# Performance work log

Hardware: AMD Instinct MI355X
Metric: run time of the kernel (lower is better)

Reference implementation:

```python
import jax, jax.numpy as jnp
import numpy as np
import math

B, T, F, H = 8, 1024, 1024, 16
D = F // H

def setup_inputs() -> dict:
    key = jax.random.key(0)
    ks = jax.random.split(key, 6)
    s = 1.0 / math.sqrt(F)
    return {
        "qkv": jax.random.normal(ks[0], (B, T, F), dtype=jnp.float32),
        "key_padding_mask": jax.random.randint(ks[1], (B, T), 0, 2).astype(bool),
        "in_proj_w": jax.random.normal(ks[2], (3 * F, F), dtype=jnp.float32) * s,
        "in_proj_b": jax.random.normal(ks[3], (3 * F,), dtype=jnp.float32) * 0.02,
        "out_proj_w": jax.random.normal(ks[4], (F, F), dtype=jnp.float32) * s,
        "out_proj_b": jax.random.normal(ks[5], (F,), dtype=jnp.float32) * 0.02,
    }

def reference(qkv, key_padding_mask, in_proj_w, in_proj_b, out_proj_w, out_proj_b):
    b, t, f = qkv.shape
    h, d = H, f // H
    norm = jnp.asarray(math.sqrt(d), dtype=qkv.dtype)
    # fused QKV projection (torch Linear: x @ W.T + b)
    x = qkv @ in_proj_w.T + in_proj_b                     # [B, T, 3F]
    q, k, v = jnp.split(x, 3, axis=-1)
    q = q.reshape(b, t, h, d).transpose(0, 2, 1, 3)       # [B, H, T, D]
    k = k.reshape(b, t, h, d).transpose(0, 2, 1, 3)
    v = v.reshape(b, t, h, d).transpose(0, 2, 1, 3)
    dot = jnp.einsum("bhqd,bhkd->bhqk", q, k) / norm      # [B, H, T, T]
    dot = jnp.where(key_padding_mask[:, None, None, :], -jnp.inf, dot)
    alpha = jax.nn.softmax(dot, axis=-1)                  # [B, H, T, T]
    att = jnp.einsum("bhqk,bhkd->bhqd", alpha, v)         # [B, H, T, D]
    att = att.transpose(0, 2, 1, 3).reshape(b, t, f)      # [B, T, F]
    out = att @ out_proj_w.T + out_proj_b
    return (out, alpha)
```

## Files before the change

### kernel.cpp

```cpp
#include <hip/hip_runtime.h>
#include <math.h>

#define B_ 8
#define T_ 1024
#define F_ 1024
#define H_ 16
#define D_ 64

typedef __bf16 bf16x8 __attribute__((ext_vector_type(8)));
typedef float f32x4 __attribute__((ext_vector_type(4)));
typedef unsigned short u16x8 __attribute__((ext_vector_type(8)));

__device__ __forceinline__ unsigned short f2bf(float f) {
    union { float f; unsigned u; } v; v.f = f;
    unsigned r = v.u + 0x7fffu + ((v.u >> 16) & 1u);
    return (unsigned short)(r >> 16);
}

__device__ __forceinline__ void gld16(const void* g, void* l) {
    __builtin_amdgcn_global_load_lds(
        (const __attribute__((address_space(1))) void*)g,
        (__attribute__((address_space(3))) void*)l, 16, 0, 0);
}

__device__ __forceinline__ int swz4(int row15) {
    return (row15 ^ (row15 >> 2)) & 3;
}

__global__ __launch_bounds__(256) void cvt3(
    const float* __restrict__ a, unsigned short* __restrict__ oa, int na8,
    const float* __restrict__ b, unsigned short* __restrict__ ob, int nb8,
    const float* __restrict__ c, unsigned short* __restrict__ oc, int nc8)
{
    int i = blockIdx.x * 256 + threadIdx.x;
    const float* in; unsigned short* out;
    if (i < na8)            { in = a; out = oa; }
    else if (i < na8 + nb8) { in = b; out = ob; i -= na8; }
    else                    { in = c; out = oc; i -= na8 + nb8; if (i >= nc8) return; }
    const float4* p = (const float4*)in + (size_t)i * 2;
    float4 x = p[0], y = p[1];
    u16x8 o;
    o[0] = f2bf(x.x); o[1] = f2bf(x.y); o[2] = f2bf(x.z); o[3] = f2bf(x.w);
    o[4] = f2bf(y.x); o[5] = f2bf(y.y); o[6] = f2bf(y.z); o[7] = f2bf(y.w);
    ((u16x8*)out)[i] = o;
}

__global__ __launch_bounds__(256) void qkv_gemm(
    const unsigned short* __restrict__ A,
    const unsigned short* __restrict__ Bw,
    const float* __restrict__ bias,
    unsigned short* __restrict__ qb,
    unsigned short* __restrict__ kb,
    unsigned short* __restrict__ vb)
{
    __shared__ __align__(16) unsigned short As[3][128 * 32];
    __shared__ __align__(16) unsigned short Bs[3][128 * 32];
    const int K = 1024;
    int tid = threadIdx.x;
    int lane = tid & 63, wave = tid >> 6;
    int wr = wave >> 1, wc = wave & 1;
    int l = blockIdx.y * 24 + blockIdx.x;
    int s = (l & 7) * 192 + (l >> 3);
    int m0 = (s / 24) * 128, n0 = (s % 24) * 128;
    int col = lane & 15, quad = lane >> 4;
    int sw = swz4(col);
    int rl = lane >> 2;
    int lc = (lane & 3) ^ swz4(rl);

    #define QKV_STAGE(ri, kt) do {                                              \
        int kc_ = (kt) * 32;                                                    \
        _Pragma("unroll")                                                       \
        for (int ld = 0; ld < 2; ld++) {                                        \
            int ia = wave * 2 + ld;                                             \
            gld16(A  + (size_t)(m0 + ia * 16 + rl) * K + kc_ + lc * 8,          \
                  &As[ri][ia * 512]);                                           \
            gld16(Bw + (size_t)(n0 + ia * 16 + rl) * K + kc_ + lc * 8,          \
                  &Bs[ri][ia * 512]);                                           \
        }                                                                       \
    } while (0)

    QKV_STAGE(0, 0);
    QKV_STAGE(1, 1);

    f32x4 acc[4][4] = {};
    int ri = 0;
    for (int t = 0; t < 31; t++) {
        asm volatile("s_waitcnt vmcnt(4)" ::: "memory");
        __builtin_amdgcn_sched_barrier(0);
        __builtin_amdgcn_s_barrier();
        bf16x8 af[4], bg[4];
        #pragma unroll
        for (int mt = 0; mt < 4; mt++)
            af[mt] = *(const bf16x8*)&As[ri][(wr * 64 + mt * 16 + col) * 32 + (quad ^ sw) * 8];
        #pragma unroll
        for (int nt = 0; nt < 4; nt++)
            bg[nt] = *(const bf16x8*)&Bs[ri][(wc * 64 + nt * 16 + col) * 32 + (quad ^ sw) * 8];
        int rn = ri + 2; if (rn >= 3) rn -= 3;
        if (t < 30) QKV_STAGE(rn, t + 2);
        #pragma unroll
        for (int mt = 0; mt < 4; mt++)
            #pragma unroll
            for (int nt = 0; nt < 4; nt++)
                acc[mt][nt] = __builtin_amdgcn_mfma_f32_16x16x32_bf16(
                    af[mt], bg[nt], acc[mt][nt], 0, 0, 0);
        ri = ri + 1; if (ri >= 3) ri -= 3;
    }
    {
        asm volatile("s_waitcnt vmcnt(0)" ::: "memory");
        __builtin_amdgcn_sched_barrier(0);
        __builtin_amdgcn_s_barrier();
        bf16x8 af[4], bg[4];
        #pragma unroll
        for (int mt = 0; mt < 4; mt++)
            af[mt] = *(const bf16x8*)&As[ri][(wr * 64 + mt * 16 + col) * 32 + (quad ^ sw) * 8];
        #pragma unroll
        for (int nt = 0; nt < 4; nt++)
            bg[nt] = *(const bf16x8*)&Bs[ri][(wc * 64 + nt * 16 + col) * 32 + (quad ^ sw) * 8];
        #pragma unroll
        for (int mt = 0; mt < 4; mt++)
            #pragma unroll
            for (int nt = 0; nt < 4; nt++)
                acc[mt][nt] = __builtin_amdgcn_mfma_f32_16x16x32_bf16(
                    af[mt], bg[nt], acc[mt][nt], 0, 0, 0);
    }
    #undef QKV_STAGE
    int which = n0 >> 10;
    #pragma unroll
    for (int nt = 0; nt < 4; nt++) {
        int n = n0 + wc * 64 + nt * 16 + col;
        int hn = (n & 1023) >> 6, d = n & 63;
        float bn = bias[n];
        #pragma unroll
        for (int mt = 0; mt < 4; mt++) {
            #pragma unroll
            for (int r = 0; r < 4; r++) {
                int m = m0 + wr * 64 + mt * 16 + quad * 4 + r;
                int bb = m >> 10, t = m & 1023;
                unsigned short bf = f2bf(acc[mt][nt][r] + bn);
                if (which == 0)
                    qb[(size_t)((bb * H_ + hn) * T_ + t) * D_ + d] = bf;
                else if (which == 1)
                    kb[(size_t)((bb * H_ + hn) * T_ + t) * D_ + d] = bf;
                else
                    vb[(size_t)((bb * H_ + hn) * D_ + d) * T_ + t] = bf;
            }
        }
    }
}

__global__ __launch_bounds__(256) void fused_attn(
    const unsigned short* __restrict__ qb,
    const unsigned short* __restrict__ kb,
    const unsigned short* __restrict__ vb,
    const int* __restrict__ mask,
    float* __restrict__ alpha,
    unsigned short* __restrict__ attb)
{
    __shared__ __align__(16) unsigned short U[16 * 1032];
    __shared__ __align__(16) unsigned short Vs[4][2][1024];
    __shared__ float redmax[4][16];
    __shared__ float redsum[4][16];
    int b = blockIdx.z, h = blockIdx.y, q0 = blockIdx.x * 16;
    int tid = threadIdx.x, lane = tid & 63, wave = tid >> 6;
    int col = lane & 15, quad = lane >> 4;
    const unsigned short* qbase = qb + ((size_t)(b * H_ + h) * T_ + q0) * D_;
    const unsigned short* kbase = kb + ((size_t)(b * H_ + h) * T_) * D_;

    bf16x8 aq0 = *(const bf16x8*)&qbase[col * 64 + quad * 8];
    bf16x8 aq1 = *(const bf16x8*)&qbase[col * 64 + 32 + quad * 8];

    int krl = lane >> 3;
    int klc = (lane & 7) ^ krl;
    int sw8 = col & 7;
    unsigned short* Kb0 = &U[wave * 4096];
    unsigned short* Kb1 = Kb0 + 2048;

    #pragma unroll
    for (int j = 0; j < 4; j++)
        gld16(kbase + (size_t)(wave * 256 + j * 8 + krl) * 64 + klc * 8, Kb0 + j * 512);
    #pragma unroll
    for (int j = 0; j < 4; j++)
        gld16(kbase + (size_t)(wave * 256 + 32 + j * 8 + krl) * 64 + klc * 8, Kb1 + j * 512);

    f32x4 acc[8][2] = {};
    #pragma unroll
    for (int it = 0; it < 8; it++) {
        if (it < 7) { asm volatile("s_waitcnt vmcnt(4)" ::: "memory"); }
        else        { asm volatile("s_waitcnt vmcnt(0)" ::: "memory"); }
        __builtin_amdgcn_sched_barrier(0);
        const unsigned short* Kb = (it & 1) ? Kb1 : Kb0;
        #pragma unroll
        for (int ct = 0; ct < 2; ct++) {
            const unsigned short* kp = Kb + (ct * 16 + col) * 64;
            bf16x8 b0 = *(const bf16x8*)&kp[(quad ^ sw8) * 8];
            bf16x8 b1 = *(const bf16x8*)&kp[((4 + quad) ^ sw8) * 8];
            acc[it][ct] = __builtin_amdgcn_mfma_f32_16x16x32_bf16(aq0, b0, acc[it][ct], 0, 0, 0);
            acc[it][ct] = __builtin_amdgcn_mfma_f32_16x16x32_bf16(aq1, b1, acc[it][ct], 0, 0, 0);
        }
        __builtin_amdgcn_sched_barrier(0);
        if (it < 6) {
            unsigned short* Kn = (it & 1) ? Kb1 : Kb0;
            #pragma unroll
            for (int j = 0; j < 4; j++)
                gld16(kbase + (size_t)(wave * 256 + (it + 2) * 32 + j * 8 + krl) * 64 + klc * 8,
                      Kn + j * 512);
        }
    }

    const unsigned short* vhead = vb + (size_t)(b * H_ + h) * D_ * T_;
    int vrl = lane >> 3;
    int vswz = (lane & 7) ^ vrl;
    #pragma unroll
    for (int i = 0; i < 2; i++)
        gld16(vhead + (size_t)(wave * 16 + i * 8 + vrl) * T_ + vswz * 8, &Vs[wave][0][i * 512]);
    #pragma unroll
    for (int i = 0; i < 2; i++)
        gld16(vhead + (size_t)(wave * 16 + i * 8 + vrl) * T_ + 64 + vswz * 8, &Vs[wave][1][i * 512]);

    const int* mrow = mask + b * T_;
    float mx[4] = {-INFINITY, -INFINITY, -INFINITY, -INFINITY};
    #pragma unroll
    for (int it = 0; it < 8; it++)
        #pragma unroll
        for (int ct = 0; ct < 2; ct++) {
            int k = wave * 256 + it * 32 + ct * 16 + col;
            bool m = mrow[k] != 0;
            #pragma unroll
            for (int r = 0; r < 4; r++) {
                float v = m ? -INFINITY : acc[it][ct][r] * 0.125f;
                acc[it][ct][r] = v;
                mx[r] = fmaxf(mx[r], v);
            }
        }
    #pragma unroll
    for (int r = 0; r < 4; r++) {
        mx[r] = fmaxf(mx[r], __shfl_xor(mx[r], 1, 64));
        mx[r] = fmaxf(mx[r], __shfl_xor(mx[r], 2, 64));
        mx[r] = fmaxf(mx[r], __shfl_xor(mx[r], 4, 64));
        mx[r] = fmaxf(mx[r], __shfl_xor(mx[r], 8, 64));
    }
    if (col == 0)
        #pragma unroll
        for (int r = 0; r < 4; r++) redmax[wave][quad * 4 + r] = mx[r];
    __syncthreads();
    float gm[4];
    #pragma unroll
    for (int r = 0; r < 4; r++) {
        int row = quad * 4 + r;
        gm[r] = fmaxf(fmaxf(redmax[0][row], redmax[1][row]),
                      fmaxf(redmax[2][row], redmax[3][row]));
    }
    float sm[4] = {0.f, 0.f, 0.f, 0.f};
    #pragma unroll
    for (int it = 0; it < 8; it++)
        #pragma unroll
        for (int ct = 0; ct < 2; ct++)
            #pragma unroll
            for (int r = 0; r < 4; r++) {
                float e = __expf(acc[it][ct][r] - gm[r]);
                acc[it][ct][r] = e;
                sm[r] += e;
            }
    #pragma unroll
    for (int r = 0; r < 4; r++) {
        sm[r] += __shfl_xor(sm[r], 1, 64);
        sm[r] += __shfl_xor(sm[r], 2, 64);
        sm[r] += __shfl_xor(sm[r], 4, 64);
        sm[r] += __shfl_xor(sm[r], 8, 64);
    }
    if (col == 0)
        #pragma unroll
        for (int r = 0; r < 4; r++) redsum[wave][quad * 4 + r] = sm[r];
    __syncthreads();
    float inv[4];
    #pragma unroll
    for (int r = 0; r < 4; r++) {
        int row = quad * 4 + r;
        inv[r] = 1.0f / (redsum[0][row] + redsum[1][row] + redsum[2][row] + redsum[3][row]);
    }
    float* abase = alpha + ((size_t)(b * H_ + h) * T_ + q0) * T_;
    #pragma unroll
    for (int it = 0; it < 8; it++)
        #pragma unroll
        for (int ct = 0; ct < 2; ct++) {
            int k = wave * 256 + it * 32 + ct * 16 + col;
            #pragma unroll
            for (int r = 0; r < 4; r++) {
                float v = acc[it][ct][r] * inv[r];
                abase[(size_t)(quad * 4 + r) * T_ + k] = v;
                U[(quad * 4 + r) * 1032 + k] = f2bf(v);
            }
        }
    __syncthreads();
    f32x4 oacc = {};
    #pragma unroll
    for (int t = 0; t < 16; t++) {
        if (t < 15) { asm volatile("s_waitcnt vmcnt(2)" ::: "memory"); }
        else        { asm volatile("s_waitcnt vmcnt(0)" ::: "memory"); }
        __builtin_amdgcn_sched_barrier(0);
        const unsigned short* Vb = Vs[wave][t & 1];
        bf16x8 pa0 = *(const bf16x8*)&U[col * 1032 + t * 64 + quad * 8];
        bf16x8 pa1 = *(const bf16x8*)&U[col * 1032 + t * 64 + 32 + quad * 8];
        bf16x8 bv0 = *(const bf16x8*)&Vb[col * 64 + ((quad ^ sw8)) * 8];
        bf16x8 bv1 = *(const bf16x8*)&Vb[col * 64 + (((quad + 4) ^ sw8)) * 8];
        oacc = __builtin_amdgcn_mfma_f32_16x16x32_bf16(pa0, bv0, oacc, 0, 0, 0);
        oacc = __builtin_amdgcn_mfma_f32_16x16x32_bf16(pa1, bv1, oacc, 0, 0, 0);
        __builtin_amdgcn_sched_barrier(0);
        if (t < 14) {
            #pragma unroll
            for (int i = 0; i < 2; i++)
                gld16(vhead + (size_t)(wave * 16 + i * 8 + vrl) * T_ + (t + 2) * 64 + vswz * 8,
                      &Vs[wave][t & 1][i * 512]);
        }
    }
    #pragma unroll
    for (int r = 0; r < 4; r++) {
        int t = q0 + quad * 4 + r;
        attb[(size_t)(b * T_ + t) * F_ + h * D_ + wave * 16 + col] = f2bf(oacc[r]);
    }
}

__global__ __launch_bounds__(256) void out_gemm(
    const unsigned short* __restrict__ A,
    const unsigned short* __restrict__ Bw,
    const float* __restrict__ bias,
    float* __restrict__ out)
{
    __shared__ __align__(16) unsigned short As[3][128 * 32];
    __shared__ __align__(16) unsigned short Bs[3][128 * 32];
    const int K = 1024;
    int tid = threadIdx.x;
    int lane = tid & 63, wave = tid >> 6;
    int wr = wave >> 1, wc = wave & 1;
    int l = blockIdx.y * 8 + blockIdx.x;
    int s = (l & 7) * 64 + (l >> 3);
    int m0 = (s / 8) * 128, n0 = (s % 8) * 128;
    int col = lane & 15, quad = lane >> 4;
    int sw = swz4(col);
    int rl = lane >> 2;
    int lc = (lane & 3) ^ swz4(rl);

    #define OUT_STAGE(ri, kt) do {                                              \
        int kc_ = (kt) * 32;                                                    \
        _Pragma("unroll")                                                       \
        for (int ld = 0; ld < 2; ld++) {                                        \
            int ia = wave * 2 + ld;                                             \
            gld16(A  + (size_t)(m0 + ia * 16 + rl) * K + kc_ + lc * 8,          \
                  &As[ri][ia * 512]);                                           \
            gld16(Bw + (size_t)(n0 + ia * 16 + rl) * K + kc_ + lc * 8,          \
                  &Bs[ri][ia * 512]);                                           \
        }                                                                       \
    } while (0)

    OUT_STAGE(0, 0);
    OUT_STAGE(1, 1);

    f32x4 acc[4][4] = {};
    int ri = 0;
    for (int t = 0; t < 31; t++) {
        asm volatile("s_waitcnt vmcnt(4)" ::: "memory");
        __builtin_amdgcn_sched_barrier(0);
        __builtin_amdgcn_s_barrier();
        bf16x8 af[4], bg[4];
        #pragma unroll
        for (int mt = 0; mt < 4; mt++)
            af[mt] = *(const bf16x8*)&As[ri][(wr * 64 + mt * 16 + col) * 32 + (quad ^ sw) * 8];
        #pragma unroll
        for (int nt = 0; nt < 4; nt++)
            bg[nt] = *(const bf16x8*)&Bs[ri][(wc * 64 + nt * 16 + col) * 32 + (quad ^ sw) * 8];
        int rn = ri + 2; if (rn >= 3) rn -= 3;
        if (t < 30) OUT_STAGE(rn, t + 2);
        #pragma unroll
        for (int mt = 0; mt < 4; mt++)
            #pragma unroll
            for (int nt = 0; nt < 4; nt++)
                acc[mt][nt] = __builtin_amdgcn_mfma_f32_16x16x32_bf16(
                    af[mt], bg[nt], acc[mt][nt], 0, 0, 0);
        ri = ri + 1; if (ri >= 3) ri -= 3;
    }
    {
        asm volatile("s_waitcnt vmcnt(0)" ::: "memory");
        __builtin_amdgcn_sched_barrier(0);
        __builtin_amdgcn_s_barrier();
        bf16x8 af[4], bg[4];
        #pragma unroll
        for (int mt = 0; mt < 4; mt++)
            af[mt] = *(const bf16x8*)&As[ri][(wr * 64 + mt * 16 + col) * 32 + (quad ^ sw) * 8];
        #pragma unroll
        for (int nt = 0; nt < 4; nt++)
            bg[nt] = *(const bf16x8*)&Bs[ri][(wc * 64 + nt * 16 + col) * 32 + (quad ^ sw) * 8];
        #pragma unroll
        for (int mt = 0; mt < 4; mt++)
            #pragma unroll
            for (int nt = 0; nt < 4; nt++)
                acc[mt][nt] = __builtin_amdgcn_mfma_f32_16x16x32_bf16(
                    af[mt], bg[nt], acc[mt][nt], 0, 0, 0);
    }
    #undef OUT_STAGE
    #pragma unroll
    for (int nt = 0; nt < 4; nt++) {
        int n = n0 + wc * 64 + nt * 16 + col;
        float bn = bias[n];
        #pragma unroll
        for (int mt = 0; mt < 4; mt++) {
            #pragma unroll
            for (int r = 0; r < 4; r++) {
                int m = m0 + wr * 64 + mt * 16 + quad * 4 + r;
                out[(size_t)m * F_ + n] = acc[mt][nt][r] + bn;
            }
        }
    }
}

extern "C" void kernel_launch(void* const* d_in, const int* in_sizes, int n_in,
                              void* d_out, int out_size, void* d_ws, size_t ws_size,
                              hipStream_t stream)
{
    const float* qkv   = (const float*)d_in[0];
    const int*   mask  = (const int*)d_in[1];
    const float* in_w  = (const float*)d_in[2];
    const float* in_b  = (const float*)d_in[3];
    const float* out_w = (const float*)d_in[4];
    const float* out_b = (const float*)d_in[5];
    float* out = (float*)d_out;
    const size_t NE = (size_t)B_ * T_ * F_;
    float* alpha = out + NE;

    unsigned short* ws   = (unsigned short*)d_ws;
    unsigned short* Xb   = ws;
    unsigned short* Wib  = Xb  + NE;
    unsigned short* Wob  = Wib + 3 * F_ * F_;
    unsigned short* qb2  = Wob + (size_t)F_ * F_;
    unsigned short* kb2  = qb2 + NE;
    unsigned short* vb2  = kb2 + NE;
    unsigned short* attb = vb2 + NE;

    const int na8 = (int)(NE / 8);
    const int nb8 = 3 * F_ * F_ / 8;
    const int nc8 = F_ * F_ / 8;
    cvt3<<<dim3((na8 + nb8 + nc8) / 256), 256, 0, stream>>>(
        qkv, Xb, na8, in_w, Wib, nb8, out_w, Wob, nc8);

    qkv_gemm<<<dim3(24, 64), 256, 0, stream>>>(Xb, Wib, in_b, qb2, kb2, vb2);
    fused_attn<<<dim3(64, H_, B_), 256, 0, stream>>>(qb2, kb2, vb2, mask, alpha, attb);
    out_gemm<<<dim3(8, 64), 256, 0, stream>>>(attb, Wob, out_b, out);
}
```

Measured before the change: 902.7 us.

## Process 32 query rows per attention block and split PV over key ranges per wave

Each attention block now handles 32 queries instead of 16, so every K tile loaded into LDS feeds two query groups and the grid halves. The PV product is restructured: each wave multiplies its own 256-key slice of probabilities against V fragments read directly from global memory, using a small per-wave LDS transpose buffer. The four per-wave partial outputs are then summed through LDS and written as vectorised bf16 stores. This removes the V LDS staging and the block-wide probability matrix, at the cost of more registers (doubled accumulators), an extra cross-wave reduction, and fewer blocks for occupancy.

```diff
diff --git a/kernel.cpp b/kernel.cpp
--- a/kernel.cpp
+++ b/kernel.cpp
@@ -157,17 +157,20 @@
     unsigned short* __restrict__ attb)
 {
     __shared__ __align__(16) unsigned short U[16 * 1032];
-    __shared__ __align__(16) unsigned short Vs[4][2][1024];
-    __shared__ float redmax[4][16];
-    __shared__ float redsum[4][16];
-    int b = blockIdx.z, h = blockIdx.y, q0 = blockIdx.x * 16;
+    __shared__ float redmax[4][32];
+    __shared__ float redsum[4][32];
+    int b = blockIdx.z, h = blockIdx.y, q0 = blockIdx.x * 32;
     int tid = threadIdx.x, lane = tid & 63, wave = tid >> 6;
     int col = lane & 15, quad = lane >> 4;
     const unsigned short* qbase = qb + ((size_t)(b * H_ + h) * T_ + q0) * D_;
     const unsigned short* kbase = kb + ((size_t)(b * H_ + h) * T_) * D_;
 
-    bf16x8 aq0 = *(const bf16x8*)&qbase[col * 64 + quad * 8];
-    bf16x8 aq1 = *(const bf16x8*)&qbase[col * 64 + 32 + quad * 8];
+    bf16x8 aq[2][2];
+    #pragma unroll
+    for (int qg = 0; qg < 2; qg++) {
+        aq[qg][0] = *(const bf16x8*)&qbase[(qg * 16 + col) * 64 + quad * 8];
+        aq[qg][1] = *(const bf16x8*)&qbase[(qg * 16 + col) * 64 + 32 + quad * 8];
+    }
 
     int krl = lane >> 3;
     int klc = (lane & 7) ^ krl;
@@ -178,11 +181,13 @@
     #pragma unroll
     for (int j = 0; j < 4; j++)
         gld16(kbase + (size_t)(wave * 256 + j * 8 + krl) * 64 + klc * 8, Kb0 + j * 512);
+    __builtin_amdgcn_sched_barrier(0);
     #pragma unroll
     for (int j = 0; j < 4; j++)
         gld16(kbase + (size_t)(wave * 256 + 32 + j * 8 + krl) * 64 + klc * 8, Kb1 + j * 512);
-
-    f32x4 acc[8][2] = {};
+    __builtin_amdgcn_sched_barrier(0);
+
+    f32x4 acc[2][8][2] = {};
     #pragma unroll
     for (int it = 0; it < 8; it++) {
         if (it < 7) { asm volatile("s_waitcnt vmcnt(4)" ::: "memory"); }
@@ -194,8 +199,13 @@
             const unsigned short* kp = Kb + (ct * 16 + col) * 64;
             bf16x8 b0 = *(const bf16x8*)&kp[(quad ^ sw8) * 8];
             bf16x8 b1 = *(const bf16x8*)&kp[((4 + quad) ^ sw8) * 8];
-            acc[it][ct] = __builtin_amdgcn_mfma_f32_16x16x32_bf16(aq0, b0, acc[it][ct], 0, 0, 0);
-            acc[it][ct] = __builtin_amdgcn_mfma_f32_16x16x32_bf16(aq1, b1, acc[it][ct], 0, 0, 0);
+            #pragma unroll
+            for (int qg = 0; qg < 2; qg++) {
+                acc[qg][it][ct] = __builtin_amdgcn_mfma_f32_16x16x32_bf16(
+                    aq[qg][0], b0, acc[qg][it][ct], 0, 0, 0);
+                acc[qg][it][ct] = __builtin_amdgcn_mfma_f32_16x16x32_bf16(
+                    aq[qg][1], b1, acc[qg][it][ct], 0, 0, 0);
+            }
         }
         __builtin_amdgcn_sched_barrier(0);
         if (it < 6) {
@@ -204,21 +214,13 @@
             for (int j = 0; j < 4; j++)
                 gld16(kbase + (size_t)(wave * 256 + (it + 2) * 32 + j * 8 + krl) * 64 + klc * 8,
                       Kn + j * 512);
-        }
-    }
-
-    const unsigned short* vhead = vb + (size_t)(b * H_ + h) * D_ * T_;
-    int vrl = lane >> 3;
-    int vswz = (lane & 7) ^ vrl;
-    #pragma unroll
-    for (int i = 0; i < 2; i++)
-        gld16(vhead + (size_t)(wave * 16 + i * 8 + vrl) * T_ + vswz * 8, &Vs[wave][0][i * 512]);
-    #pragma unroll
-    for (int i = 0; i < 2; i++)
-        gld16(vhead + (size_t)(wave * 16 + i * 8 + vrl) * T_ + 64 + vswz * 8, &Vs[wave][1][i * 512]);
+            __builtin_amdgcn_sched_barrier(0);
+        }
+    }
 
     const int* mrow = mask + b * T_;
-    float mx[4] = {-INFINITY, -INFINITY, -INFINITY, -INFINITY};
+    float mx[2][4] = {{-INFINITY, -INFINITY, -INFINITY, -INFINITY},
+                      {-INFINITY, -INFINITY, -INFINITY, -INFINITY}};
     #pragma unroll
     for (int it = 0; it < 8; it++)
         #pragma unroll
@@ -226,97 +228,149 @@
             int k = wave * 256 + it * 32 + ct * 16 + col;
             bool m = mrow[k] != 0;
             #pragma unroll
-            for (int r = 0; r < 4; r++) {
-                float v = m ? -INFINITY : acc[it][ct][r] * 0.125f;
-                acc[it][ct][r] = v;
-                mx[r] = fmaxf(mx[r], v);
-            }
-        }
-    #pragma unroll
-    for (int r = 0; r < 4; r++) {
-        mx[r] = fmaxf(mx[r], __shfl_xor(mx[r], 1, 64));
-        mx[r] = fmaxf(mx[r], __shfl_xor(mx[r], 2, 64));
-        mx[r] = fmaxf(mx[r], __shfl_xor(mx[r], 4, 64));
-        mx[r] = fmaxf(mx[r], __shfl_xor(mx[r], 8, 64));
-    }
+            for (int qg = 0; qg < 2; qg++)
+                #pragma unroll
+                for (int r = 0; r < 4; r++) {
+                    float v = m ? -INFINITY : acc[qg][it][ct][r] * 0.125f;
+                    acc[qg][it][ct][r] = v;
+                    mx[qg][r] = fmaxf(mx[qg][r], v);
+                }
+        }
+    #pragma unroll
+    for (int qg = 0; qg < 2; qg++)
+        #pragma unroll
+        for (int r = 0; r < 4; r++) {
+            mx[qg][r] = fmaxf(mx[qg][r], __shfl_xor(mx[qg][r], 1, 64));
+            mx[qg][r] = fmaxf(mx[qg][r], __shfl_xor(mx[qg][r], 2, 64));
+            mx[qg][r] = fmaxf(mx[qg][r], __shfl_xor(mx[qg][r], 4, 64));
+            mx[qg][r] = fmaxf(mx[qg][r], __shfl_xor(mx[qg][r], 8, 64));
+        }
     if (col == 0)
         #pragma unroll
-        for (int r = 0; r < 4; r++) redmax[wave][quad * 4 + r] = mx[r];
+        for (int qg = 0; qg < 2; qg++)
+            #pragma unroll
+            for (int r = 0; r < 4; r++)
+                redmax[wave][qg * 16 + quad * 4 + r] = mx[qg][r];
     __syncthreads();
-    float gm[4];
-    #pragma unroll
-    for (int r = 0; r < 4; r++) {
-        int row = quad * 4 + r;
-        gm[r] = fmaxf(fmaxf(redmax[0][row], redmax[1][row]),
-                      fmaxf(redmax[2][row], redmax[3][row]));
-    }
-    float sm[4] = {0.f, 0.f, 0.f, 0.f};
+    float gm[2][4];
+    #pragma unroll
+    for (int qg = 0; qg < 2; qg++)
+        #pragma unroll
+        for (int r = 0; r < 4; r++) {
+            int row = qg * 16 + quad * 4 + r;
+            gm[qg][r] = fmaxf(fmaxf(redmax[0][row], redmax[1][row]),
+                              fmaxf(redmax[2][row], redmax[3][row]));
+        }
+    float sm[2][4] = {};
     #pragma unroll
     for (int it = 0; it < 8; it++)
         #pragma unroll
         for (int ct = 0; ct < 2; ct++)
             #pragma unroll
-            for (int r = 0; r < 4; r++) {
-                float e = __expf(acc[it][ct][r] - gm[r]);
-                acc[it][ct][r] = e;
-                sm[r] += e;
-            }
-    #pragma unroll
-    for (int r = 0; r < 4; r++) {
-        sm[r] += __shfl_xor(sm[r], 1, 64);
-        sm[r] += __shfl_xor(sm[r], 2, 64);
-        sm[r] += __shfl_xor(sm[r], 4, 64);
-        sm[r] += __shfl_xor(sm[r], 8, 64);
-    }
+            for (int qg = 0; qg < 2; qg++)
+                #pragma unroll
+                for (int r = 0; r < 4; r++) {
+                    float e = __expf(acc[qg][it][ct][r] - gm[qg][r]);
+                    acc[qg][it][ct][r] = e;
+                    sm[qg][r] += e;
+                }
+    #pragma unroll
+    for (int qg = 0; qg < 2; qg++)
+        #pragma unroll
+        for (int r = 0; r < 4; r++) {
+            sm[qg][r] += __shfl_xor(sm[qg][r], 1, 64);
+            sm[qg][r] += __shfl_xor(sm[qg][r], 2, 64);
+            sm[qg][r] += __shfl_xor(sm[qg][r], 4, 64);
+            sm[qg][r] += __shfl_xor(sm[qg][r], 8, 64);
+        }
     if (col == 0)
         #pragma unroll
-        for (int r = 0; r < 4; r++) redsum[wave][quad * 4 + r] = sm[r];
+        for (int qg = 0; qg < 2; qg++)
+            #pragma unroll
+            for (int r = 0; r < 4; r++)
+                redsum[wave][qg * 16 + quad * 4 + r] = sm[qg][r];
     __syncthreads();
-    float inv[4];
-    #pragma unroll
-    for (int r = 0; r < 4; r++) {
-        int row = quad * 4 + r;
-        inv[r] = 1.0f / (redsum[0][row] + redsum[1][row] + redsum[2][row] + redsum[3][row]);
-    }
+    float inv[2][4];
+    #pragma unroll
+    for (int qg = 0; qg < 2; qg++)
+        #pragma unroll
+        for (int r = 0; r < 4; r++) {
+            int row = qg * 16 + quad * 4 + r;
+            inv[qg][r] = 1.0f / (redsum[0][row] + redsum[1][row] +
+                                 redsum[2][row] + redsum[3][row]);
+        }
+
     float* abase = alpha + ((size_t)(b * H_ + h) * T_ + q0) * T_;
-    #pragma unroll
-    for (int it = 0; it < 8; it++)
+    const unsigned short* vhead = vb + (size_t)(b * H_ + h) * D_ * T_;
+    unsigned short* tbuf = &U[wave * 4096];
+    f32x4 oacc[2][4] = {};
+    bf16x8 bfr[4];
+    {
+        int t0 = wave * 256;
+        #pragma unroll
+        for (int dt = 0; dt < 4; dt++)
+            bfr[dt] = *(const bf16x8*)&vhead[(size_t)(dt * 16 + col) * T_ + t0 + quad * 8];
+    }
+    #pragma unroll
+    for (int it = 0; it < 8; it++) {
+        int t0 = wave * 256 + it * 32;
         #pragma unroll
         for (int ct = 0; ct < 2; ct++) {
-            int k = wave * 256 + it * 32 + ct * 16 + col;
-            #pragma unroll
-            for (int r = 0; r < 4; r++) {
-                float v = acc[it][ct][r] * inv[r];
-                abase[(size_t)(quad * 4 + r) * T_ + k] = v;
-                U[(quad * 4 + r) * 1032 + k] = f2bf(v);
-            }
-        }
+            int k = t0 + ct * 16 + col;
+            #pragma unroll
+            for (int qg = 0; qg < 2; qg++)
+                #pragma unroll
+                for (int r = 0; r < 4; r++) {
+                    float v = acc[qg][it][ct][r] * inv[qg][r];
+                    int q = qg * 16 + quad * 4 + r;
+                    abase[(size_t)q * T_ + k] = v;
+                    tbuf[q * 40 + ct * 16 + col] = f2bf(v);
+                }
+        }
+        bf16x8 bfn[4];
+        if (it < 7) {
+            int t1 = t0 + 32;
+            #pragma unroll
+            for (int dt = 0; dt < 4; dt++)
+                bfn[dt] = *(const bf16x8*)&vhead[(size_t)(dt * 16 + col) * T_ + t1 + quad * 8];
+        }
+        asm volatile("s_waitcnt lgkmcnt(0)" ::: "memory");
+        __builtin_amdgcn_sched_barrier(0);
+        bf16x8 afr[2];
+        #pragma unroll
+        for (int qg = 0; qg < 2; qg++)
+            afr[qg] = *(const bf16x8*)&tbuf[(qg * 16 + col) * 40 + quad * 8];
+        #pragma unroll
+        for (int qg = 0; qg < 2; qg++)
+            #pragma unroll
+            for (int dt = 0; dt < 4; dt++)
+                oacc[qg][dt] = __builtin_amdgcn_mfma_f32_16x16x32_bf16(
+                    afr[qg], bfr[dt], oacc[qg][dt], 0, 0, 0);
+        __builtin_amdgcn_sched_barrier(0);
+        if (it < 7) {
+            #pragma unroll
+            for (int dt = 0; dt < 4; dt++) bfr[dt] = bfn[dt];
+        }
+    }
+    float* Ow = (float*)U + wave * 2048;
+    #pragma unroll
+    for (int qg = 0; qg < 2; qg++)
+        #pragma unroll
+        for (int dt = 0; dt < 4; dt++)
+            #pragma unroll
+            for (int r = 0; r < 4; r++)
+                Ow[(qg * 16 + quad * 4 + r) * 64 + dt * 16 + col] = oacc[qg][dt][r];
     __syncthreads();
-    f32x4 oacc = {};
-    #pragma unroll
-    for (int t = 0; t < 16; t++) {
-        if (t < 15) { asm volatile("s_waitcnt vmcnt(2)" ::: "memory"); }
-        else        { asm volatile("s_waitcnt vmcnt(0)" ::: "memory"); }
-        __builtin_amdgcn_sched_barrier(0);
-        const unsigned short* Vb = Vs[wave][t & 1];
-        bf16x8 pa0 = *(const bf16x8*)&U[col * 1032 + t * 64 + quad * 8];
-        bf16x8 pa1 = *(const bf16x8*)&U[col * 1032 + t * 64 + 32 + quad * 8];
-        bf16x8 bv0 = *(const bf16x8*)&Vb[col * 64 + ((quad ^ sw8)) * 8];
-        bf16x8 bv1 = *(const bf16x8*)&Vb[col * 64 + (((quad + 4) ^ sw8)) * 8];
-        oacc = __builtin_amdgcn_mfma_f32_16x16x32_bf16(pa0, bv0, oacc, 0, 0, 0);
-        oacc = __builtin_amdgcn_mfma_f32_16x16x32_bf16(pa1, bv1, oacc, 0, 0, 0);
-        __builtin_amdgcn_sched_barrier(0);
-        if (t < 14) {
-            #pragma unroll
-            for (int i = 0; i < 2; i++)
-                gld16(vhead + (size_t)(wave * 16 + i * 8 + vrl) * T_ + (t + 2) * 64 + vswz * 8,
-                      &Vs[wave][t & 1][i * 512]);
-        }
-    }
-    #pragma unroll
-    for (int r = 0; r < 4; r++) {
-        int t = q0 + quad * 4 + r;
-        attb[(size_t)(b * T_ + t) * F_ + h * D_ + wave * 16 + col] = f2bf(oacc[r]);
+    {
+        int q = tid >> 3, dg = tid & 7;
+        const float* O0 = (const float*)U;
+        u16x8 o;
+        #pragma unroll
+        for (int j = 0; j < 8; j++) {
+            int idx = q * 64 + dg * 8 + j;
+            o[j] = f2bf(O0[idx] + O0[2048 + idx] + O0[4096 + idx] + O0[6144 + idx]);
+        }
+        *(u16x8*)&attb[(size_t)(b * T_ + q0 + q) * F_ + h * D_ + dg * 8] = o;
     }
 }
 
@@ -442,6 +496,6 @@
         qkv, Xb, na8, in_w, Wib, nb8, out_w, Wob, nc8);
 
     qkv_gemm<<<dim3(24, 64), 256, 0, stream>>>(Xb, Wib, in_b, qb2, kb2, vb2);
-    fused_attn<<<dim3(64, H_, B_), 256, 0, stream>>>(qb2, kb2, vb2, mask, alpha, attb);
+    fused_attn<<<dim3(32, H_, B_), 256, 0, stream>>>(qb2, kb2, vb2, mask, alpha, attb);
     out_gemm<<<dim3(8, 64), 256, 0, stream>>>(attb, Wob, out_b, out);
 }
```

Result: no change. 897.6 us (-0.6%).
